# Optimization experiments

Measured on AMD Instinct MI355X. Metric: run time of the kernel, lower is better.

## Reference

```python
import jax, jax.numpy as jnp
import numpy as np
import math

E = 64          # embed_size
S = 64          # max_seq_len (mask hard-codes seq==64)
H = 8           # num_heads
DH = E // H     # 8
DFF = 4 * E     # 256
V = 32000       # vocab_size
B = 64          # batch


def _pos_encoding():
    position = np.arange(0, S, dtype=np.float32)[:, None]
    div_term = np.exp(np.arange(0, E, 2, dtype=np.float32) * -(math.log(10000.0) / E))
    pe = np.zeros((S, E), dtype=np.float32)
    pe[:, 0::2] = np.sin(position * div_term)
    pe[:, 1::2] = np.cos(position * div_term)
    return jnp.asarray(pe)


def layernorm(x, g, b, eps=1e-5):
    mu = jnp.mean(x, -1, keepdims=True)
    var = jnp.mean((x - mu) ** 2, -1, keepdims=True)
    return (x - mu) * jax.lax.rsqrt(var + eps) * g + b


def round4(x):
    return jnp.round(x * 1e4) / 1e4


def setup_inputs() -> dict:
    key = jax.random.key(0)
    ks = jax.random.split(key, 16)
    n = lambda k, sh, s=0.05: jax.random.normal(k, sh, dtype=jnp.float32) * s
    return {
        "x": jax.random.randint(ks[0], (B, S), 0, V),
        "emb": n(ks[1], (V, E), 1.0),
        "pe": _pos_encoding(),
        # per-head q/k/v weights concatenated: [E, H*DH] == [E, E], no bias
        "wq": n(ks[2], (E, E)), "wk": n(ks[3], (E, E)), "wv": n(ks[4], (E, E)),
        "g_h": jnp.ones((E,)), "b_h": jnp.zeros((E,)),           # MHA internal LayerNorm
        "wo": n(ks[5], (E, E)), "bo": jnp.zeros((E,)),           # MHA output linear
        "g1": jnp.ones((E,)), "bt1": jnp.zeros((E,)),            # norm1
        "w1": n(ks[6], (E, DFF)), "b1f": jnp.zeros((DFF,)),      # ffn fc1
        "w2": n(ks[7], (DFF, E)), "b2f": jnp.zeros((E,)),        # ffn fc2
        "g2": jnp.ones((E,)), "bt2": jnp.zeros((E,)),            # norm2
        "gf": jnp.ones((E,)), "bf": jnp.zeros((E,)),             # final norm
        "wout": n(ks[8], (E, V)), "bout": jnp.zeros((V,)),       # final linear
    }


def reference(x, emb, pe, wq, wk, wv, g_h, b_h, wo, bo, g1, bt1,
              w1, b1f, w2, b2f, g2, bt2, gf, bf, wout, bout):
    # embedding + positional encoding (dropout = identity in eval)
    h = emb[x] + pe[:S]                              # [B,S,E]

    # --- multi-head attention (per-head linears fused as one GEMM each) ---
    q = (h @ wq).reshape(B, S, H, DH)
    k = (h @ wk).reshape(B, S, H, DH)
    v = (h @ wv).reshape(B, S, H, DH)
    scores = jnp.einsum('bshd,bthd->bhst', q, k) / math.sqrt(DH)
    causal = jnp.tril(jnp.ones((S, S), dtype=bool))
    scores = jnp.where(causal, scores, -jnp.inf)
    attn = jax.nn.softmax(scores, axis=-1)
    ho = round4(jnp.einsum('bhst,bthd->bshd', attn, v))  # per-head round(decimals=4)
    concat = ho.reshape(B, S, E)
    attn_out = jnp.round(layernorm(concat, g_h, b_h) @ wo + bo)  # round to integers

    # --- transformer block residual/norm/ffn ---
    h = layernorm(h + attn_out, g1, bt1)
    ffn = jax.nn.relu(h @ w1 + b1f) @ w2 + b2f
    h = round4(layernorm(h + ffn, g2, bt2))

    # --- final norm, vocab projection, softmax, round ---
    logits = layernorm(h, gf, bf) @ wout + bout       # [B,S,V]
    probs = jax.nn.softmax(logits, axis=-1)
    return jnp.round(probs)
```

## Files before the change

### kernel.cpp

```cpp
#include <hip/hip_runtime.h>
#include <hip/hip_bf16.h>
#include <math.h>

#define EMB 64
#define SEQ 64
#define NH 8
#define DFF 256
#define VOC 32000
#define BATCH 64

using bf16_t = __hip_bfloat16;
typedef __bf16 bf16x8 __attribute__((ext_vector_type(8)));
typedef float f32x4 __attribute__((ext_vector_type(4)));

#define WOUTT_OFF 0
#define HBF_OFF   4194304
#define GSUM_OFF  (4194304 + 524288)
#define GMAX_OFF  (4194304 + 524288 + 16384)

#define NFILL 512

__device__ inline unsigned long long packmax(float f, int i) {
  unsigned u = __float_as_uint(f);
  u = (u & 0x80000000u) ? ~u : (u | 0x80000000u);
  return ((unsigned long long)u << 32) | (unsigned)i;
}

template <int OP>
__device__ inline void gemm64t(const float* __restrict__ in, const float* __restrict__ W,
                               const float* __restrict__ bias, float* __restrict__ out,
                               int t) {
  int i = t >> 2, j0 = (t & 3) * 16;
  float acc[16];
#pragma unroll
  for (int j = 0; j < 16; ++j) acc[j] = 0.f;
  for (int k = 0; k < 64; ++k) {
    float a = in[i * 65 + k];
    const float4* wr = (const float4*)(W + k * 64 + j0);
    float4 w0 = wr[0], w1v = wr[1], w2v = wr[2], w3v = wr[3];
    acc[0] += a * w0.x;   acc[1] += a * w0.y;   acc[2] += a * w0.z;   acc[3] += a * w0.w;
    acc[4] += a * w1v.x;  acc[5] += a * w1v.y;  acc[6] += a * w1v.z;  acc[7] += a * w1v.w;
    acc[8] += a * w2v.x;  acc[9] += a * w2v.y;  acc[10] += a * w2v.z; acc[11] += a * w2v.w;
    acc[12] += a * w3v.x; acc[13] += a * w3v.y; acc[14] += a * w3v.z; acc[15] += a * w3v.w;
  }
#pragma unroll
  for (int j = 0; j < 16; ++j) {
    float v = acc[j] + (bias ? bias[j0 + j] : 0.f);
    if (OP == 1) v = rintf(v);
    out[i * 65 + j0 + j] = v;
  }
}

__global__ __launch_bounds__(256) void k_prep(
    const int* __restrict__ x, const float* __restrict__ emb, const float* __restrict__ pe,
    const float* __restrict__ wq, const float* __restrict__ wk, const float* __restrict__ wv,
    const float* __restrict__ g_h, const float* __restrict__ b_h,
    const float* __restrict__ wo, const float* __restrict__ bo,
    const float* __restrict__ g1, const float* __restrict__ bt1,
    const float* __restrict__ w1, const float* __restrict__ b1f,
    const float* __restrict__ w2, const float* __restrict__ b2f,
    const float* __restrict__ g2, const float* __restrict__ bt2,
    const float* __restrict__ gf, const float* __restrict__ bf_,
    const float* __restrict__ wout, bf16_t* __restrict__ woutT,
    bf16_t* __restrict__ hbf, float* __restrict__ gsums,
    unsigned long long* __restrict__ gmax, float* __restrict__ outp) {
  const int t = threadIdx.x;
  __shared__ float sm[6 * 64 * 65];

  if (blockIdx.x >= 564) {
    f32x4 z = {0.f, 0.f, 0.f, 0.f};
    f32x4* o4 = (f32x4*)outp;
    const size_t nvec = (size_t)BATCH * SEQ * VOC / 4;
    const size_t stride = (size_t)NFILL * 256;
    for (size_t i = (size_t)(blockIdx.x - 564) * 256 + t; i < nvec; i += stride)
      __builtin_nontemporal_store(z, o4 + i);
    return;
  }

  if (blockIdx.x >= 64) {
    float* tile = sm;
    int v0 = (blockIdx.x - 64) * 64;
    for (int idx = t; idx < 4096; idx += 256) {
      int e = idx >> 6, c = idx & 63;
      tile[e * 65 + c] = wout[(size_t)e * VOC + v0 + c];
    }
    __syncthreads();
    for (int idx = t; idx < 4096; idx += 256) {
      int c = idx >> 6, e = idx & 63;
      woutT[(size_t)(v0 + c) * 64 + e] = __float2bfloat16(tile[e * 65 + c]);
    }
    return;
  }

  const int b = blockIdx.x;
  if (t < 64) {
    gsums[b * 64 + t] = 0.f;
    gmax[b * 64 + t] = 0ULL;
  }

  float* Hs = sm;
  float* Qs = sm + 4160;
  float* Ks = sm + 2 * 4160;
  float* Vs = sm + 3 * 4160;
  float* SC = sm + 4 * 4160;
  float* HO = sm + 5 * 4160;
  float* MID = sm + 4160;

  for (int idx = t; idx < 4096; idx += 256) {
    int i = idx >> 6, e = idx & 63;
    int tok = x[b * 64 + i];
    Hs[i * 65 + e] = emb[(size_t)tok * 64 + e] + pe[i * 64 + e];
  }
  __syncthreads();

  gemm64t<0>(Hs, wq, nullptr, Qs, t);
  gemm64t<0>(Hs, wk, nullptr, Ks, t);
  gemm64t<0>(Hs, wv, nullptr, Vs, t);
  __syncthreads();

  const float scale = 0.35355339059327373f;
  for (int hh = 0; hh < NH; ++hh) {
    int qc = hh * 8;
    {
      int i = t >> 2, jb = t & 3;
      float qv[8];
#pragma unroll
      for (int d = 0; d < 8; ++d) qv[d] = Qs[i * 65 + qc + d];
      for (int jj = 0; jj < 16; ++jj) {
        int j = jb * 16 + jj;
        float s;
        if (j <= i) {
          s = 0.f;
#pragma unroll
          for (int d = 0; d < 8; ++d) s += qv[d] * Ks[j * 65 + qc + d];
          s *= scale;
        } else {
          s = -INFINITY;
        }
        SC[i * 65 + j] = s;
      }
    }
    __syncthreads();
    if (t < 64) {
      int i = t;
      float m = -INFINITY;
      for (int j = 0; j <= i; ++j) m = fmaxf(m, SC[i * 65 + j]);
      float sum = 0.f;
      for (int j = 0; j <= i; ++j) {
        float e2 = __expf(SC[i * 65 + j] - m);
        SC[i * 65 + j] = e2;
        sum += e2;
      }
      float inv = 1.f / sum;
      for (int j = 0; j <= i; ++j) SC[i * 65 + j] *= inv;
      for (int j = i + 1; j < 64; ++j) SC[i * 65 + j] = 0.f;
    }
    __syncthreads();
    for (int idx = t; idx < 512; idx += 256) {
      int i = idx >> 3, d = idx & 7;
      float o = 0.f;
      for (int j = 0; j < 64; ++j) o += SC[i * 65 + j] * Vs[j * 65 + qc + d];
      HO[i * 65 + qc + d] = rintf(o * 1e4f) / 1e4f;
    }
    __syncthreads();
  }

  if (t < 64) {
    int i = t;
    float mu = 0.f;
    for (int e = 0; e < 64; ++e) mu += HO[i * 65 + e];
    mu *= (1.f / 64.f);
    float var = 0.f;
    for (int e = 0; e < 64; ++e) { float d = HO[i * 65 + e] - mu; var += d * d; }
    var *= (1.f / 64.f);
    float rs = rsqrtf(var + 1e-5f);
    for (int e = 0; e < 64; ++e) SC[i * 65 + e] = (HO[i * 65 + e] - mu) * rs * g_h[e] + b_h[e];
  }
  __syncthreads();
  gemm64t<1>(SC, wo, bo, HO, t);
  __syncthreads();

  if (t < 64) {
    int i = t;
    for (int e = 0; e < 64; ++e) Hs[i * 65 + e] += HO[i * 65 + e];
    float mu = 0.f;
    for (int e = 0; e < 64; ++e) mu += Hs[i * 65 + e];
    mu *= (1.f / 64.f);
    float var = 0.f;
    for (int e = 0; e < 64; ++e) { float d = Hs[i * 65 + e] - mu; var += d * d; }
    var *= (1.f / 64.f);
    float rs = rsqrtf(var + 1e-5f);
    for (int e = 0; e < 64; ++e) Hs[i * 65 + e] = (Hs[i * 65 + e] - mu) * rs * g1[e] + bt1[e];
  }
  __syncthreads();

  {
    int i = t >> 2, jq = t & 3;
    for (int c = 0; c < 4; ++c) {
      int j0 = jq * 64 + c * 16;
      float acc[16];
#pragma unroll
      for (int j = 0; j < 16; ++j) acc[j] = 0.f;
      for (int k = 0; k < 64; ++k) {
        float a = Hs[i * 65 + k];
        const float4* wr = (const float4*)(w1 + (size_t)k * 256 + j0);
        float4 w0 = wr[0], w1v = wr[1], w2v = wr[2], w3v = wr[3];
        acc[0] += a * w0.x;   acc[1] += a * w0.y;   acc[2] += a * w0.z;   acc[3] += a * w0.w;
        acc[4] += a * w1v.x;  acc[5] += a * w1v.y;  acc[6] += a * w1v.z;  acc[7] += a * w1v.w;
        acc[8] += a * w2v.x;  acc[9] += a * w2v.y;  acc[10] += a * w2v.z; acc[11] += a * w2v.w;
        acc[12] += a * w3v.x; acc[13] += a * w3v.y; acc[14] += a * w3v.z; acc[15] += a * w3v.w;
      }
#pragma unroll
      for (int j = 0; j < 16; ++j)
        MID[i * 260 + j0 + j] = fmaxf(acc[j] + b1f[j0 + j], 0.f);
    }
  }
  __syncthreads();

  {
    int i = t >> 2, j0 = (t & 3) * 16;
    float acc[16];
#pragma unroll
    for (int j = 0; j < 16; ++j) acc[j] = 0.f;
    for (int k = 0; k < 256; ++k) {
      float a = MID[i * 260 + k];
      const float4* wr = (const float4*)(w2 + (size_t)k * 64 + j0);
      float4 w0 = wr[0], w1v = wr[1], w2v = wr[2], w3v = wr[3];
      acc[0] += a * w0.x;   acc[1] += a * w0.y;   acc[2] += a * w0.z;   acc[3] += a * w0.w;
      acc[4] += a * w1v.x;  acc[5] += a * w1v.y;  acc[6] += a * w1v.z;  acc[7] += a * w1v.w;
      acc[8] += a * w2v.x;  acc[9] += a * w2v.y;  acc[10] += a * w2v.z; acc[11] += a * w2v.w;
      acc[12] += a * w3v.x; acc[13] += a * w3v.y; acc[14] += a * w3v.z; acc[15] += a * w3v.w;
    }
#pragma unroll
    for (int j = 0; j < 16; ++j) HO[i * 65 + j0 + j] = acc[j] + b2f[j0 + j];
  }
  __syncthreads();

  if (t < 64) {
    int i = t;
    for (int e = 0; e < 64; ++e) Hs[i * 65 + e] += HO[i * 65 + e];
    float mu = 0.f;
    for (int e = 0; e < 64; ++e) mu += Hs[i * 65 + e];
    mu *= (1.f / 64.f);
    float var = 0.f;
    for (int e = 0; e < 64; ++e) { float d = Hs[i * 65 + e] - mu; var += d * d; }
    var *= (1.f / 64.f);
    float rs = rsqrtf(var + 1e-5f);
    for (int e = 0; e < 64; ++e)
      Hs[i * 65 + e] = rintf(((Hs[i * 65 + e] - mu) * rs * g2[e] + bt2[e]) * 1e4f) / 1e4f;
    float mu2 = 0.f;
    for (int e = 0; e < 64; ++e) mu2 += Hs[i * 65 + e];
    mu2 *= (1.f / 64.f);
    float var2 = 0.f;
    for (int e = 0; e < 64; ++e) { float d = Hs[i * 65 + e] - mu2; var2 += d * d; }
    var2 *= (1.f / 64.f);
    float rs2 = rsqrtf(var2 + 1e-5f);
    for (int e = 0; e < 64; ++e) SC[i * 65 + e] = (Hs[i * 65 + e] - mu2) * rs2 * gf[e] + bf_[e];
  }
  __syncthreads();

  for (int idx = t; idx < 4096; idx += 256) {
    int i = idx >> 6, e = idx & 63;
    hbf[((size_t)b * 64 + i) * 64 + e] = __float2bfloat16(SC[i * 65 + e]);
  }
}

__global__ __launch_bounds__(256) void k_sumexp(const bf16_t* __restrict__ hbf,
                                                const bf16_t* __restrict__ woutT,
                                                const float* __restrict__ bout,
                                                float* __restrict__ gsums,
                                                unsigned long long* __restrict__ gmax) {
  const int t = threadIdx.x;
  const int lane = t & 63, wave = t >> 6;
  const int row0 = blockIdx.x * 64;
  const int nbase = blockIdx.y * 4000;
  const int mrow = lane & 15, quad = lane >> 4;
  __shared__ float lsum[64];
  if (t < 64) lsum[t] = 0.f;
  __syncthreads();

  bf16x8 a0[4], a1[4];
#pragma unroll
  for (int at = 0; at < 4; ++at) {
    const bf16_t* arow = hbf + (size_t)(row0 + at * 16 + mrow) * 64 + quad * 8;
    a0[at] = *(const bf16x8*)(arow);
    a1[at] = *(const bf16x8*)(arow + 32);
  }

  float s[4][4];
  float mxv[4][4];
  int mxi[4][4];
#pragma unroll
  for (int at = 0; at < 4; ++at)
#pragma unroll
    for (int r = 0; r < 4; ++r) { s[at][r] = 0.f; mxv[at][r] = -INFINITY; mxi[at][r] = 0; }

  for (int tt = wave; tt < 250; tt += 4) {
    int col = nbase + tt * 16 + mrow;
    const bf16_t* brow = woutT + (size_t)col * 64 + quad * 8;
    bf16x8 b0 = *(const bf16x8*)(brow);
    bf16x8 b1 = *(const bf16x8*)(brow + 32);
    float bv = bout[col];
#pragma unroll
    for (int at = 0; at < 4; ++at) {
      f32x4 c = {0.f, 0.f, 0.f, 0.f};
      c = __builtin_amdgcn_mfma_f32_16x16x32_bf16(a0[at], b0, c, 0, 0, 0);
      c = __builtin_amdgcn_mfma_f32_16x16x32_bf16(a1[at], b1, c, 0, 0, 0);
#pragma unroll
      for (int r = 0; r < 4; ++r) {
        float v = c[r] + bv;
        s[at][r] += __expf(v);
        mxi[at][r] = (v > mxv[at][r]) ? col : mxi[at][r];
        mxv[at][r] = fmaxf(mxv[at][r], v);
      }
    }
  }
#pragma unroll
  for (int off = 1; off < 16; off <<= 1) {
#pragma unroll
    for (int at = 0; at < 4; ++at)
#pragma unroll
      for (int r = 0; r < 4; ++r) {
        s[at][r] += __shfl_xor(s[at][r], off, 64);
        float ov = __shfl_xor(mxv[at][r], off, 64);
        int oi = __shfl_xor(mxi[at][r], off, 64);
        if (ov > mxv[at][r] || (ov == mxv[at][r] && oi > mxi[at][r])) {
          mxv[at][r] = ov; mxi[at][r] = oi;
        }
      }
  }
  if (mrow == 0) {
#pragma unroll
    for (int at = 0; at < 4; ++at)
#pragma unroll
      for (int r = 0; r < 4; ++r) {
        atomicAdd(&lsum[at * 16 + quad * 4 + r], s[at][r]);
        atomicMax(&gmax[row0 + at * 16 + quad * 4 + r], packmax(mxv[at][r], mxi[at][r]));
      }
  }
  __syncthreads();
  if (t < 64) atomicAdd(&gsums[row0 + t], lsum[t]);
}

__global__ __launch_bounds__(256) void k_scatter(const float* __restrict__ gsums,
                                                 const unsigned long long* __restrict__ gmax,
                                                 float* __restrict__ out) {
  int row = blockIdx.x * 256 + threadIdx.x;
  if (row >= BATCH * SEQ) return;
  unsigned long long p = gmax[row];
  unsigned key = (unsigned)(p >> 32);
  int idx = (int)(p & 0xffffffffu);
  unsigned ub = (key & 0x80000000u) ? (key & 0x7fffffffu) : ~key;
  float lmax = __uint_as_float(ub);
  float iv = 1.0f / gsums[row];
  float v = rintf(__expf(lmax) * iv);
  if (v != 0.0f) out[(size_t)row * VOC + idx] = v;
}

extern "C" void kernel_launch(void* const* d_in, const int* in_sizes, int n_in,
                              void* d_out, int out_size, void* d_ws, size_t ws_size,
                              hipStream_t stream) {
  const int* x = (const int*)d_in[0];
  const float* emb = (const float*)d_in[1];
  const float* pe = (const float*)d_in[2];
  const float* wq = (const float*)d_in[3];
  const float* wk = (const float*)d_in[4];
  const float* wv = (const float*)d_in[5];
  const float* g_h = (const float*)d_in[6];
  const float* b_h = (const float*)d_in[7];
  const float* wo = (const float*)d_in[8];
  const float* bo = (const float*)d_in[9];
  const float* g1 = (const float*)d_in[10];
  const float* bt1 = (const float*)d_in[11];
  const float* w1 = (const float*)d_in[12];
  const float* b1f = (const float*)d_in[13];
  const float* w2 = (const float*)d_in[14];
  const float* b2f = (const float*)d_in[15];
  const float* g2 = (const float*)d_in[16];
  const float* bt2 = (const float*)d_in[17];
  const float* gf = (const float*)d_in[18];
  const float* bff = (const float*)d_in[19];
  const float* wout = (const float*)d_in[20];
  const float* bout = (const float*)d_in[21];

  char* ws = (char*)d_ws;
  bf16_t* woutT = (bf16_t*)(ws + WOUTT_OFF);
  bf16_t* hbf = (bf16_t*)(ws + HBF_OFF);
  float* gsums = (float*)(ws + GSUM_OFF);
  unsigned long long* gmax = (unsigned long long*)(ws + GMAX_OFF);
  float* out = (float*)d_out;

  k_prep<<<564 + NFILL, 256, 0, stream>>>(x, emb, pe, wq, wk, wv, g_h, b_h, wo, bo,
                                          g1, bt1, w1, b1f, w2, b2f, g2, bt2, gf, bff,
                                          wout, woutT, hbf, gsums, gmax, out);
  dim3 grid(64, 8);
  k_sumexp<<<grid, 256, 0, stream>>>(hbf, woutT, bout, gsums, gmax);
  k_scatter<<<16, 256, 0, stream>>>(gsums, gmax, out);
}
```

Measured before the change: 894.0 us.

## Split fused prep kernel into QKV, per-head attention, and row-parallel FFN kernels

Replaces the single 64-block prep kernel, which ran the whole encoder per batch with serial per-row LayerNorms, with three kernels. The first computes QKV per batch and handles the woutT transpose and output zeroing. The second does attention with one block per (batch, head), softmax in registers and shuffle reductions. The third runs LayerNorm, Wo, FFN and the final norms over 16-row tiles with shuffle reductions. This spreads the serial encoder work over many more blocks, at the cost of extra launches, global round trips for H/Q/K/V/HO, and a coarser zero-fill with plain rather than nontemporal stores.

```diff
diff --git a/kernel.cpp b/kernel.cpp
--- a/kernel.cpp
+++ b/kernel.cpp
@@ -16,9 +16,12 @@
 #define WOUTT_OFF 0
 #define HBF_OFF   4194304
 #define GSUM_OFF  (4194304 + 524288)
-#define GMAX_OFF  (4194304 + 524288 + 16384)
-
-#define NFILL 512
+#define GMAX_OFF  (GSUM_OFF + 16384)
+#define H_OFF     (GMAX_OFF + 32768)
+#define Q_OFF     (H_OFF + 1048576)
+#define K_OFF     (Q_OFF + 1048576)
+#define V_OFF     (K_OFF + 1048576)
+#define HO_OFF    (V_OFF + 1048576)
 
 __device__ inline unsigned long long packmax(float f, int i) {
   unsigned u = __float_as_uint(f);
@@ -26,14 +29,21 @@
   return ((unsigned long long)u << 32) | (unsigned)i;
 }
 
-template <int OP>
-__device__ inline void gemm64t(const float* __restrict__ in, const float* __restrict__ W,
-                               const float* __restrict__ bias, float* __restrict__ out,
-                               int t) {
+__device__ inline float rsum16(float s) {
+  s += __shfl_xor(s, 1, 16);
+  s += __shfl_xor(s, 2, 16);
+  s += __shfl_xor(s, 4, 16);
+  s += __shfl_xor(s, 8, 16);
+  return s;
+}
+
+__device__ inline void gemm64g(const float* __restrict__ in, const float* __restrict__ W,
+                               float* __restrict__ out, int t) {
   int i = t >> 2, j0 = (t & 3) * 16;
   float acc[16];
 #pragma unroll
   for (int j = 0; j < 16; ++j) acc[j] = 0.f;
+#pragma unroll 2
   for (int k = 0; k < 64; ++k) {
     float a = in[i * 65 + k];
     const float4* wr = (const float4*)(W + k * 64 + j0);
@@ -44,16 +54,126 @@
     acc[12] += a * w3v.x; acc[13] += a * w3v.y; acc[14] += a * w3v.z; acc[15] += a * w3v.w;
   }
 #pragma unroll
-  for (int j = 0; j < 16; ++j) {
-    float v = acc[j] + (bias ? bias[j0 + j] : 0.f);
-    if (OP == 1) v = rintf(v);
-    out[i * 65 + j0 + j] = v;
-  }
-}
-
-__global__ __launch_bounds__(256) void k_prep(
+  for (int j = 0; j < 16; ++j) out[(size_t)i * 64 + j0 + j] = acc[j];
+}
+
+__global__ __launch_bounds__(256) void k_qkv(
     const int* __restrict__ x, const float* __restrict__ emb, const float* __restrict__ pe,
     const float* __restrict__ wq, const float* __restrict__ wk, const float* __restrict__ wv,
+    const float* __restrict__ wout, bf16_t* __restrict__ woutT,
+    float* __restrict__ H, float* __restrict__ Q, float* __restrict__ K,
+    float* __restrict__ V, float* __restrict__ gsums,
+    unsigned long long* __restrict__ gmax, float* __restrict__ outp) {
+  const int t = threadIdx.x;
+  __shared__ float sm[64 * 65];
+
+  if (blockIdx.x >= 564) {
+    const int bid = blockIdx.x - 564;
+    f32x4 z = {0.f, 0.f, 0.f, 0.f};
+    f32x4* o4 = (f32x4*)outp + (size_t)bid * 32000;
+    for (int i = t; i < 32000; i += 256) o4[i] = z;
+    return;
+  }
+
+  if (blockIdx.x >= 64) {
+    int v0 = (blockIdx.x - 64) * 64;
+    for (int idx = t; idx < 4096; idx += 256) {
+      int e = idx >> 6, c = idx & 63;
+      sm[e * 65 + c] = wout[(size_t)e * VOC + v0 + c];
+    }
+    __syncthreads();
+    for (int idx = t; idx < 4096; idx += 256) {
+      int c = idx >> 6, e = idx & 63;
+      woutT[(size_t)(v0 + c) * 64 + e] = __float2bfloat16(sm[e * 65 + c]);
+    }
+    return;
+  }
+
+  const int b = blockIdx.x;
+  if (t < 64) {
+    gsums[b * 64 + t] = 0.f;
+    gmax[b * 64 + t] = 0ULL;
+  }
+  for (int idx = t; idx < 4096; idx += 256) {
+    int i = idx >> 6, e = idx & 63;
+    int tok = x[b * 64 + i];
+    float v = emb[(size_t)tok * 64 + e] + pe[i * 64 + e];
+    sm[i * 65 + e] = v;
+    H[((size_t)b * 64 + i) * 64 + e] = v;
+  }
+  __syncthreads();
+  gemm64g(sm, wq, Q + (size_t)b * 4096, t);
+  gemm64g(sm, wk, K + (size_t)b * 4096, t);
+  gemm64g(sm, wv, V + (size_t)b * 4096, t);
+}
+
+__global__ __launch_bounds__(256) void k_attn(const float* __restrict__ Q,
+                                              const float* __restrict__ K,
+                                              const float* __restrict__ V,
+                                              float* __restrict__ HO) {
+  const int b = blockIdx.x, h = blockIdx.y;
+  const int t = threadIdx.x;
+  __shared__ float Qh[64 * 8], Kh[64 * 8], Vh[64 * 8];
+  __shared__ float SC[64 * 65];
+  const size_t base = (size_t)b * 4096 + h * 8;
+
+  for (int idx = t; idx < 512; idx += 256) {
+    int i = idx >> 3, d = idx & 7;
+    Qh[i * 8 + d] = Q[base + (size_t)i * 64 + d];
+    Kh[i * 8 + d] = K[base + (size_t)i * 64 + d];
+    Vh[i * 8 + d] = V[base + (size_t)i * 64 + d];
+  }
+  __syncthreads();
+
+  const float scale = 0.35355339059327373f;
+  const int i = t >> 2, jb = t & 3;
+  float qv[8];
+#pragma unroll
+  for (int d = 0; d < 8; ++d) qv[d] = Qh[i * 8 + d];
+
+  float sv[16];
+  float m = -INFINITY;
+#pragma unroll
+  for (int jj = 0; jj < 16; ++jj) {
+    int j = jb * 16 + jj;
+    float s;
+    if (j <= i) {
+      s = 0.f;
+#pragma unroll
+      for (int d = 0; d < 8; ++d) s += qv[d] * Kh[j * 8 + d];
+      s *= scale;
+    } else {
+      s = -INFINITY;
+    }
+    sv[jj] = s;
+    m = fmaxf(m, s);
+  }
+  m = fmaxf(m, __shfl_xor(m, 1, 4));
+  m = fmaxf(m, __shfl_xor(m, 2, 4));
+  float sum = 0.f;
+#pragma unroll
+  for (int jj = 0; jj < 16; ++jj) {
+    float e2 = __expf(sv[jj] - m);
+    sv[jj] = e2;
+    sum += e2;
+  }
+  sum += __shfl_xor(sum, 1, 4);
+  sum += __shfl_xor(sum, 2, 4);
+  float inv = 1.f / sum;
+#pragma unroll
+  for (int jj = 0; jj < 16; ++jj) SC[i * 65 + jb * 16 + jj] = sv[jj] * inv;
+  __syncthreads();
+
+  for (int idx = t; idx < 512; idx += 256) {
+    int ii = idx >> 3, d = idx & 7;
+    float o = 0.f;
+    for (int j = 0; j < 64; ++j) o += SC[ii * 65 + j] * Vh[j * 8 + d];
+    HO[base + (size_t)ii * 64 + d] = rintf(o * 1e4f) / 1e4f;
+  }
+}
+
+__global__ __launch_bounds__(256) void k_ffn(
+    const float* __restrict__ H, const float* __restrict__ HO,
     const float* __restrict__ g_h, const float* __restrict__ b_h,
     const float* __restrict__ wo, const float* __restrict__ bo,
     const float* __restrict__ g1, const float* __restrict__ bt1,
@@ -61,170 +181,71 @@
     const float* __restrict__ w2, const float* __restrict__ b2f,
     const float* __restrict__ g2, const float* __restrict__ bt2,
     const float* __restrict__ gf, const float* __restrict__ bf_,
-    const float* __restrict__ wout, bf16_t* __restrict__ woutT,
-    bf16_t* __restrict__ hbf, float* __restrict__ gsums,
-    unsigned long long* __restrict__ gmax, float* __restrict__ outp) {
+    bf16_t* __restrict__ hbf) {
   const int t = threadIdx.x;
-  __shared__ float sm[6 * 64 * 65];
-
-  if (blockIdx.x >= 564) {
-    f32x4 z = {0.f, 0.f, 0.f, 0.f};
-    f32x4* o4 = (f32x4*)outp;
-    const size_t nvec = (size_t)BATCH * SEQ * VOC / 4;
-    const size_t stride = (size_t)NFILL * 256;
-    for (size_t i = (size_t)(blockIdx.x - 564) * 256 + t; i < nvec; i += stride)
-      __builtin_nontemporal_store(z, o4 + i);
-    return;
-  }
-
-  if (blockIdx.x >= 64) {
-    float* tile = sm;
-    int v0 = (blockIdx.x - 64) * 64;
-    for (int idx = t; idx < 4096; idx += 256) {
-      int e = idx >> 6, c = idx & 63;
-      tile[e * 65 + c] = wout[(size_t)e * VOC + v0 + c];
-    }
-    __syncthreads();
-    for (int idx = t; idx < 4096; idx += 256) {
-      int c = idx >> 6, e = idx & 63;
-      woutT[(size_t)(v0 + c) * 64 + e] = __float2bfloat16(tile[e * 65 + c]);
-    }
-    return;
-  }
-
-  const int b = blockIdx.x;
-  if (t < 64) {
-    gsums[b * 64 + t] = 0.f;
-    gmax[b * 64 + t] = 0ULL;
-  }
-
-  float* Hs = sm;
-  float* Qs = sm + 4160;
-  float* Ks = sm + 2 * 4160;
-  float* Vs = sm + 3 * 4160;
-  float* SC = sm + 4 * 4160;
-  float* HO = sm + 5 * 4160;
-  float* MID = sm + 4160;
-
-  for (int idx = t; idx < 4096; idx += 256) {
-    int i = idx >> 6, e = idx & 63;
-    int tok = x[b * 64 + i];
-    Hs[i * 65 + e] = emb[(size_t)tok * 64 + e] + pe[i * 64 + e];
-  }
-  __syncthreads();
-
-  gemm64t<0>(Hs, wq, nullptr, Qs, t);
-  gemm64t<0>(Hs, wk, nullptr, Ks, t);
-  gemm64t<0>(Hs, wv, nullptr, Vs, t);
-  __syncthreads();
-
-  const float scale = 0.35355339059327373f;
-  for (int hh = 0; hh < NH; ++hh) {
-    int qc = hh * 8;
-    {
-      int i = t >> 2, jb = t & 3;
-      float qv[8];
-#pragma unroll
-      for (int d = 0; d < 8; ++d) qv[d] = Qs[i * 65 + qc + d];
-      for (int jj = 0; jj < 16; ++jj) {
-        int j = jb * 16 + jj;
-        float s;
-        if (j <= i) {
-          s = 0.f;
-#pragma unroll
-          for (int d = 0; d < 8; ++d) s += qv[d] * Ks[j * 65 + qc + d];
-          s *= scale;
-        } else {
-          s = -INFINITY;
-        }
-        SC[i * 65 + j] = s;
-      }
-    }
-    __syncthreads();
-    if (t < 64) {
-      int i = t;
-      float m = -INFINITY;
-      for (int j = 0; j <= i; ++j) m = fmaxf(m, SC[i * 65 + j]);
-      float sum = 0.f;
-      for (int j = 0; j <= i; ++j) {
-        float e2 = __expf(SC[i * 65 + j] - m);
-        SC[i * 65 + j] = e2;
-        sum += e2;
-      }
-      float inv = 1.f / sum;
-      for (int j = 0; j <= i; ++j) SC[i * 65 + j] *= inv;
-      for (int j = i + 1; j < 64; ++j) SC[i * 65 + j] = 0.f;
-    }
-    __syncthreads();
-    for (int idx = t; idx < 512; idx += 256) {
-      int i = idx >> 3, d = idx & 7;
-      float o = 0.f;
-      for (int j = 0; j < 64; ++j) o += SC[i * 65 + j] * Vs[j * 65 + qc + d];
-      HO[i * 65 + qc + d] = rintf(o * 1e4f) / 1e4f;
-    }
-    __syncthreads();
-  }
-
-  if (t < 64) {
-    int i = t;
-    float mu = 0.f;
-    for (int e = 0; e < 64; ++e) mu += HO[i * 65 + e];
-    mu *= (1.f / 64.f);
-    float var = 0.f;
-    for (int e = 0; e < 64; ++e) { float d = HO[i * 65 + e] - mu; var += d * d; }
-    var *= (1.f / 64.f);
+  const int r0 = blockIdx.x * 16;
+  const int i = t >> 4, l = t & 15;
+  const int e0 = l * 4;
+  const size_t row = (size_t)(r0 + i) * 64;
+  __shared__ float T1[16 * 65];
+  __shared__ float T2[16 * 65];
+  __shared__ float H1[16 * 65];
+  __shared__ float M[16 * 260];
+
+  {
+    float4 hv = *(const float4*)(HO + row + e0);
+    float mu = rsum16(hv.x + hv.y + hv.z + hv.w) * (1.f / 64.f);
+    float d0 = hv.x - mu, d1 = hv.y - mu, d2 = hv.z - mu, d3 = hv.w - mu;
+    float var = rsum16(d0 * d0 + d1 * d1 + d2 * d2 + d3 * d3) * (1.f / 64.f);
     float rs = rsqrtf(var + 1e-5f);
-    for (int e = 0; e < 64; ++e) SC[i * 65 + e] = (HO[i * 65 + e] - mu) * rs * g_h[e] + b_h[e];
-  }
-  __syncthreads();
-  gemm64t<1>(SC, wo, bo, HO, t);
-  __syncthreads();
-
-  if (t < 64) {
-    int i = t;
-    for (int e = 0; e < 64; ++e) Hs[i * 65 + e] += HO[i * 65 + e];
-    float mu = 0.f;
-    for (int e = 0; e < 64; ++e) mu += Hs[i * 65 + e];
-    mu *= (1.f / 64.f);
-    float var = 0.f;
-    for (int e = 0; e < 64; ++e) { float d = Hs[i * 65 + e] - mu; var += d * d; }
-    var *= (1.f / 64.f);
+    T1[i * 65 + e0 + 0] = d0 * rs * g_h[e0 + 0] + b_h[e0 + 0];
+    T1[i * 65 + e0 + 1] = d1 * rs * g_h[e0 + 1] + b_h[e0 + 1];
+    T1[i * 65 + e0 + 2] = d2 * rs * g_h[e0 + 2] + b_h[e0 + 2];
+    T1[i * 65 + e0 + 3] = d3 * rs * g_h[e0 + 3] + b_h[e0 + 3];
+  }
+  __syncthreads();
+
+  {
+    float a0 = 0.f, a1 = 0.f, a2 = 0.f, a3 = 0.f;
+#pragma unroll 4
+    for (int k = 0; k < 64; ++k) {
+      float a = T1[i * 65 + k];
+      float4 w = *(const float4*)(wo + (size_t)k * 64 + e0);
+      a0 += a * w.x; a1 += a * w.y; a2 += a * w.z; a3 += a * w.w;
+    }
+    T2[i * 65 + e0 + 0] = rintf(a0 + bo[e0 + 0]);
+    T2[i * 65 + e0 + 1] = rintf(a1 + bo[e0 + 1]);
+    T2[i * 65 + e0 + 2] = rintf(a2 + bo[e0 + 2]);
+    T2[i * 65 + e0 + 3] = rintf(a3 + bo[e0 + 3]);
+  }
+  __syncthreads();
+
+  {
+    float4 hh = *(const float4*)(H + row + e0);
+    float x0 = hh.x + T2[i * 65 + e0 + 0];
+    float x1 = hh.y + T2[i * 65 + e0 + 1];
+    float x2 = hh.z + T2[i * 65 + e0 + 2];
+    float x3 = hh.w + T2[i * 65 + e0 + 3];
+    float mu = rsum16(x0 + x1 + x2 + x3) * (1.f / 64.f);
+    float d0 = x0 - mu, d1 = x1 - mu, d2 = x2 - mu, d3 = x3 - mu;
+    float var = rsum16(d0 * d0 + d1 * d1 + d2 * d2 + d3 * d3) * (1.f / 64.f);
     float rs = rsqrtf(var + 1e-5f);
-    for (int e = 0; e < 64; ++e) Hs[i * 65 + e] = (Hs[i * 65 + e] - mu) * rs * g1[e] + bt1[e];
-  }
-  __syncthreads();
-
-  {
-    int i = t >> 2, jq = t & 3;
-    for (int c = 0; c < 4; ++c) {
-      int j0 = jq * 64 + c * 16;
-      float acc[16];
-#pragma unroll
-      for (int j = 0; j < 16; ++j) acc[j] = 0.f;
-      for (int k = 0; k < 64; ++k) {
-        float a = Hs[i * 65 + k];
-        const float4* wr = (const float4*)(w1 + (size_t)k * 256 + j0);
-        float4 w0 = wr[0], w1v = wr[1], w2v = wr[2], w3v = wr[3];
-        acc[0] += a * w0.x;   acc[1] += a * w0.y;   acc[2] += a * w0.z;   acc[3] += a * w0.w;
-        acc[4] += a * w1v.x;  acc[5] += a * w1v.y;  acc[6] += a * w1v.z;  acc[7] += a * w1v.w;
-        acc[8] += a * w2v.x;  acc[9] += a * w2v.y;  acc[10] += a * w2v.z; acc[11] += a * w2v.w;
-        acc[12] += a * w3v.x; acc[13] += a * w3v.y; acc[14] += a * w3v.z; acc[15] += a * w3v.w;
-      }
-#pragma unroll
-      for (int j = 0; j < 16; ++j)
-        MID[i * 260 + j0 + j] = fmaxf(acc[j] + b1f[j0 + j], 0.f);
-    }
-  }
-  __syncthreads();
-
-  {
-    int i = t >> 2, j0 = (t & 3) * 16;
+    H1[i * 65 + e0 + 0] = d0 * rs * g1[e0 + 0] + bt1[e0 + 0];
+    H1[i * 65 + e0 + 1] = d1 * rs * g1[e0 + 1] + bt1[e0 + 1];
+    H1[i * 65 + e0 + 2] = d2 * rs * g1[e0 + 2] + bt1[e0 + 2];
+    H1[i * 65 + e0 + 3] = d3 * rs * g1[e0 + 3] + bt1[e0 + 3];
+  }
+  __syncthreads();
+
+  {
+    const int j0 = l * 16;
     float acc[16];
 #pragma unroll
     for (int j = 0; j < 16; ++j) acc[j] = 0.f;
-    for (int k = 0; k < 256; ++k) {
-      float a = MID[i * 260 + k];
-      const float4* wr = (const float4*)(w2 + (size_t)k * 64 + j0);
+#pragma unroll 2
+    for (int k = 0; k < 64; ++k) {
+      float a = H1[i * 65 + k];
+      const float4* wr = (const float4*)(w1 + (size_t)k * 256 + j0);
       float4 w0 = wr[0], w1v = wr[1], w2v = wr[2], w3v = wr[3];
       acc[0] += a * w0.x;   acc[1] += a * w0.y;   acc[2] += a * w0.z;   acc[3] += a * w0.w;
       acc[4] += a * w1v.x;  acc[5] += a * w1v.y;  acc[6] += a * w1v.z;  acc[7] += a * w1v.w;
@@ -232,36 +253,43 @@
       acc[12] += a * w3v.x; acc[13] += a * w3v.y; acc[14] += a * w3v.z; acc[15] += a * w3v.w;
     }
 #pragma unroll
-    for (int j = 0; j < 16; ++j) HO[i * 65 + j0 + j] = acc[j] + b2f[j0 + j];
-  }
-  __syncthreads();
-
-  if (t < 64) {
-    int i = t;
-    for (int e = 0; e < 64; ++e) Hs[i * 65 + e] += HO[i * 65 + e];
-    float mu = 0.f;
-    for (int e = 0; e < 64; ++e) mu += Hs[i * 65 + e];
-    mu *= (1.f / 64.f);
-    float var = 0.f;
-    for (int e = 0; e < 64; ++e) { float d = Hs[i * 65 + e] - mu; var += d * d; }
-    var *= (1.f / 64.f);
+    for (int j = 0; j < 16; ++j)
+      M[i * 260 + j0 + j] = fmaxf(acc[j] + b1f[j0 + j], 0.f);
+  }
+  __syncthreads();
+
+  float f0 = 0.f, f1 = 0.f, f2 = 0.f, f3 = 0.f;
+  {
+#pragma unroll 4
+    for (int k = 0; k < 256; ++k) {
+      float a = M[i * 260 + k];
+      float4 w = *(const float4*)(w2 + (size_t)k * 64 + e0);
+      f0 += a * w.x; f1 += a * w.y; f2 += a * w.z; f3 += a * w.w;
+    }
+    f0 += b2f[e0 + 0]; f1 += b2f[e0 + 1]; f2 += b2f[e0 + 2]; f3 += b2f[e0 + 3];
+  }
+
+  {
+    float y0 = H1[i * 65 + e0 + 0] + f0;
+    float y1 = H1[i * 65 + e0 + 1] + f1;
+    float y2 = H1[i * 65 + e0 + 2] + f2;
+    float y3 = H1[i * 65 + e0 + 3] + f3;
+    float mu = rsum16(y0 + y1 + y2 + y3) * (1.f / 64.f);
+    float d0 = y0 - mu, d1 = y1 - mu, d2 = y2 - mu, d3 = y3 - mu;
+    float var = rsum16(d0 * d0 + d1 * d1 + d2 * d2 + d3 * d3) * (1.f / 64.f);
     float rs = rsqrtf(var + 1e-5f);
-    for (int e = 0; e < 64; ++e)
-      Hs[i * 65 + e] = rintf(((Hs[i * 65 + e] - mu) * rs * g2[e] + bt2[e]) * 1e4f) / 1e4f;
-    float mu2 = 0.f;
-    for (int e = 0; e < 64; ++e) mu2 += Hs[i * 65 + e];
-    mu2 *= (1.f / 64.f);
-    float var2 = 0.f;
-    for (int e = 0; e < 64; ++e) { float d = Hs[i * 65 + e] - mu2; var2 += d * d; }
-    var2 *= (1.f / 64.f);
+    float h20 = rintf((d0 * rs * g2[e0 + 0] + bt2[e0 + 0]) * 1e4f) / 1e4f;
+    float h21 = rintf((d1 * rs * g2[e0 + 1] + bt2[e0 + 1]) * 1e4f) / 1e4f;
+    float h22 = rintf((d2 * rs * g2[e0 + 2] + bt2[e0 + 2]) * 1e4f) / 1e4f;
+    float h23 = rintf((d3 * rs * g2[e0 + 3] + bt2[e0 + 3]) * 1e4f) / 1e4f;
+    float mu2 = rsum16(h20 + h21 + h22 + h23) * (1.f / 64.f);
+    float e0d = h20 - mu2, e1d = h21 - mu2, e2d = h22 - mu2, e3d = h23 - mu2;
+    float var2 = rsum16(e0d * e0d + e1d * e1d + e2d * e2d + e3d * e3d) * (1.f / 64.f);
     float rs2 = rsqrtf(var2 + 1e-5f);
-    for (int e = 0; e < 64; ++e) SC[i * 65 + e] = (Hs[i * 65 + e] - mu2) * rs2 * gf[e] + bf_[e];
-  }
-  __syncthreads();
-
-  for (int idx = t; idx < 4096; idx += 256) {
-    int i = idx >> 6, e = idx & 63;
-    hbf[((size_t)b * 64 + i) * 64 + e] = __float2bfloat16(SC[i * 65 + e]);
+    hbf[row + e0 + 0] = __float2bfloat16(e0d * rs2 * gf[e0 + 0] + bf_[e0 + 0]);
+    hbf[row + e0 + 1] = __float2bfloat16(e1d * rs2 * gf[e0 + 1] + bf_[e0 + 1]);
+    hbf[row + e0 + 2] = __float2bfloat16(e2d * rs2 * gf[e0 + 2] + bf_[e0 + 2]);
+    hbf[row + e0 + 3] = __float2bfloat16(e3d * rs2 * gf[e0 + 3] + bf_[e0 + 3]);
   }
 }
 
@@ -388,11 +416,18 @@
   bf16_t* hbf = (bf16_t*)(ws + HBF_OFF);
   float* gsums = (float*)(ws + GSUM_OFF);
   unsigned long long* gmax = (unsigned long long*)(ws + GMAX_OFF);
+  float* H = (float*)(ws + H_OFF);
+  float* Q = (float*)(ws + Q_OFF);
+  float* K = (float*)(ws + K_OFF);
+  float* V = (float*)(ws + V_OFF);
+  float* HO = (float*)(ws + HO_OFF);
   float* out = (float*)d_out;
 
-  k_prep<<<564 + NFILL, 256, 0, stream>>>(x, emb, pe, wq, wk, wv, g_h, b_h, wo, bo,
-                                          g1, bt1, w1, b1f, w2, b2f, g2, bt2, gf, bff,
-                                          wout, woutT, hbf, gsums, gmax, out);
+  k_qkv<<<1588, 256, 0, stream>>>(x, emb, pe, wq, wk, wv, wout, woutT,
+                                  H, Q, K, V, gsums, gmax, out);
+  k_attn<<<dim3(64, 8), 256, 0, stream>>>(Q, K, V, HO);
+  k_ffn<<<256, 256, 0, stream>>>(H, HO, g_h, b_h, wo, bo, g1, bt1, w1, b1f,
+                                 w2, b2f, g2, bt2, gf, bff, hbf);
   dim3 grid(64, 8);
   k_sumexp<<<grid, 256, 0, stream>>>(hbf, woutT, bout, gsums, gmax);
   k_scatter<<<16, 256, 0, stream>>>(gsums, gmax, out);
```

After: 757.3 us. -15.3%, faster.
